# Kernel tuning notes

Hardware: AMD Instinct MI355X
Metric: run time of the kernel (lower is better)

## Reference

```python
import jax, jax.numpy as jnp
import numpy as np

N = 4096
TAU = 0.2          # args.tau relaxation temperature
EPS = 1e-10        # numerical guard for logit of clamped probs


def setup_inputs() -> dict:
    key = jax.random.key(0)
    k1, k2, k3 = jax.random.split(key, 3)
    r = jax.random.uniform(k1, (N, N))
    ori_adj = jnp.where(r < 0.005, -1.0, jnp.where(r < 0.01, 1.0, 0.0)).astype(jnp.float32)
    # nn.init.uniform_(change_links_prob, 0.0, 0.001)
    change_links_prob = jax.random.uniform(k2, (N, N), minval=0.0, maxval=0.001, dtype=jnp.float32)
    # uniform noise for the RelaxedBernoulli logistic reparameterization
    u = jax.random.uniform(k3, (N, N), minval=1e-6, maxval=1.0 - 1e-6, dtype=jnp.float32)
    return {"ori_adj": ori_adj, "change_links_prob": change_links_prob, "u": u}


def reference(ori_adj, change_links_prob, u):
    # --- get_modified_adj: RelaxedBernoulliStraightThrough(tau, clamp(p,0,1)).rsample() ---
    p = jnp.clip(change_links_prob, EPS, 1.0 - EPS)      # torch.clamp(p, 0, 1) + logit guard
    logits = jnp.log(p) - jnp.log1p(-p)
    noise = jnp.log(u) - jnp.log1p(-u)                   # logistic noise
    soft = jax.nn.sigmoid((logits + noise) / TAU)        # relaxed sample
    hard = jnp.round(soft)                               # quantized sample
    change_prob = soft + jax.lax.stop_gradient(hard - soft)  # straight-through
    mod_adj = ori_adj + change_prob * (-2.0 * ori_adj)   # ori_adj * (1 - 2*b)

    # --- balance_degree_directed(mod_adj) ---
    # torch.diag(matrix) returns the diagonal VECTOR, broadcast-subtracted per row (faithful).
    A = mod_adj + mod_adj.T - jnp.diag(mod_adj)
    A_abs = jnp.abs(A)
    tr3 = jnp.einsum('ij,jk,ki->', A, A, A)              # trace(A @ A @ A)
    tr3_abs = jnp.einsum('ij,jk,ki->', A_abs, A_abs, A_abs)
    balance = 0.5 * (1.0 + tr3 / tr3_abs)
    return mod_adj, balance
```

## Files before the change

### kernel.cpp

```cpp
#include <hip/hip_runtime.h>
#include <hip/hip_bf16.h>
#include <cstdint>
#include <cstddef>

#define N 4096
#define NN ((size_t)N * (size_t)N)

typedef int int4v  __attribute__((ext_vector_type(4)));
typedef int int16v __attribute__((ext_vector_type(16)));

__device__ inline void async16(const void* g, void* lds) {
    __builtin_amdgcn_global_load_lds(
        (const __attribute__((address_space(1))) void*)g,
        (__attribute__((address_space(3))) void*)lds, 16, 0, 0);
}

__device__ __noinline__ float mod_full(float p_raw, float uu, float o) {
    float p = fminf(fmaxf(p_raw, 1e-10f), 1.0f - 1e-10f);
    float logits = logf(p) - log1pf(-p);
    float noise  = logf(uu) - log1pf(-uu);
    float y = (logits + noise) / 0.2f;
    float soft = 1.0f / (1.0f + expf(-y));
    float hard = rintf(soft);
    return o + hard * (-2.0f * o);
}

__device__ inline float mod_elem(float p_raw, float uu, float o) {
    float p = fmaxf(p_raw, 1e-10f);
    float s = p + uu;
    if (__builtin_expect(fabsf(s - 1.0f) < 1e-5f, 0))
        return mod_full(p_raw, uu, o);
    return (s > 1.0f) ? -o : o;
}

__global__ void diag_kernel(const float* __restrict__ ori, const float* __restrict__ clp,
                            const float* __restrict__ u, float* __restrict__ diag,
                            double* __restrict__ accs) {
    int j = blockIdx.x * blockDim.x + threadIdx.x;
    size_t idx = (size_t)j * N + j;
    diag[j] = mod_elem(clp[idx], u[idx], ori[idx]);
    if (blockIdx.x == 0 && threadIdx.x < 2) accs[threadIdx.x] = 0.0;
}

__device__ inline int pk4(const int* v) {
    return (v[0] & 255) | ((v[1] & 255) << 8) | ((v[2] & 255) << 16) | ((v[3] & 255) << 24);
}
__device__ inline int pk4a(const int* v) {
    int a0 = v[0] < 0 ? -v[0] : v[0], a1 = v[1] < 0 ? -v[1] : v[1];
    int a2 = v[2] < 0 ? -v[2] : v[2], a3 = v[3] < 0 ? -v[3] : v[3];
    return a0 | (a1 << 8) | (a2 << 16) | (a3 << 24);
}

__global__ __launch_bounds__(256) void fused_mod_A(
        const float* __restrict__ ori, const float* __restrict__ clp,
        const float* __restrict__ u, const float* __restrict__ diag,
        float* __restrict__ out,
        signed char* __restrict__ A, signed char* __restrict__ AT,
        signed char* __restrict__ Aa, signed char* __restrict__ ATa) {
    const int bx = blockIdx.x, by = blockIdx.y;
    if (bx > by) return;
    const bool dg = (bx == by);
    const int bi = bx * 64, bj = by * 64;
    __shared__ float mij[64][68];
    __shared__ float mji[64][68];
    __shared__ float dj_s[64], di_s[64];
    const int t = threadIdx.x;
    const int r = t >> 2;
    const int c16 = (t & 3) << 4;
    if (t < 64) dj_s[t] = diag[bj + t];
    else if (t < 128) di_s[t - 64] = diag[bi + t - 64];
    {
        const size_t base = (size_t)(bi + r) * N + bj + c16;
        #pragma unroll
        for (int q = 0; q < 4; ++q) {
            const size_t idx = base + q * 4;
            float4 p4 = *(const float4*)&clp[idx];
            float4 u4 = *(const float4*)&u[idx];
            float4 o4 = *(const float4*)&ori[idx];
            float4 m4;
            m4.x = mod_elem(p4.x, u4.x, o4.x);
            m4.y = mod_elem(p4.y, u4.y, o4.y);
            m4.z = mod_elem(p4.z, u4.z, o4.z);
            m4.w = mod_elem(p4.w, u4.w, o4.w);
            *(float4*)&out[idx] = m4;
            *(float4*)&mij[r][c16 + q * 4] = m4;
        }
    }
    if (!dg) {
        const size_t base = (size_t)(bj + r) * N + bi + c16;
        #pragma unroll
        for (int q = 0; q < 4; ++q) {
            const size_t idx = base + q * 4;
            float4 p4 = *(const float4*)&clp[idx];
            float4 u4 = *(const float4*)&u[idx];
            float4 o4 = *(const float4*)&ori[idx];
            float4 m4;
            m4.x = mod_elem(p4.x, u4.x, o4.x);
            m4.y = mod_elem(p4.y, u4.y, o4.y);
            m4.z = mod_elem(p4.z, u4.z, o4.z);
            m4.w = mod_elem(p4.w, u4.w, o4.w);
            *(float4*)&out[idx] = m4;
            *(float4*)&mji[r][c16 + q * 4] = m4;
        }
    }
    __syncthreads();
    float (*Mji)[68] = dg ? mij : mji;
    int aF[16], tF[16], aM[16], tM[16];
    const float djr = dj_s[r], dir = di_s[r];
    #pragma unroll
    for (int k = 0; k < 16; ++k) {
        const int c = c16 + k;
        const float x  = mij[r][c];
        const float xt = mij[c][r];
        const float y  = Mji[r][c];
        const float yt = Mji[c][r];
        aF[k] = (int)(x + yt - dj_s[c]);
        tF[k] = (int)(xt + y - djr);
        if (!dg) {
            aM[k] = (int)(y + xt - di_s[c]);
            tM[k] = (int)(yt + x - dir);
        }
    }
    const size_t oF = (size_t)(bi + r) * N + bj + c16;
    const size_t oM = (size_t)(bj + r) * N + bi + c16;
    *(int4*)&A  [oF] = make_int4(pk4 (aF), pk4 (aF + 4), pk4 (aF + 8), pk4 (aF + 12));
    *(int4*)&Aa [oF] = make_int4(pk4a(aF), pk4a(aF + 4), pk4a(aF + 8), pk4a(aF + 12));
    *(int4*)&AT [oM] = make_int4(pk4 (tF), pk4 (tF + 4), pk4 (tF + 8), pk4 (tF + 12));
    *(int4*)&ATa[oM] = make_int4(pk4a(tF), pk4a(tF + 4), pk4a(tF + 8), pk4a(tF + 12));
    if (!dg) {
        *(int4*)&A  [oM] = make_int4(pk4 (aM), pk4 (aM + 4), pk4 (aM + 8), pk4 (aM + 12));
        *(int4*)&Aa [oM] = make_int4(pk4a(aM), pk4a(aM + 4), pk4a(aM + 8), pk4a(aM + 12));
        *(int4*)&AT [oF] = make_int4(pk4 (tM), pk4 (tM + 4), pk4 (tM + 8), pk4 (tM + 12));
        *(int4*)&ATa[oF] = make_int4(pk4a(tM), pk4a(tM + 4), pk4a(tM + 8), pk4a(tM + 12));
    }
}

__global__ __launch_bounds__(256) void gemm_trace_i8(const signed char* __restrict__ Ag,
                                                     const signed char* __restrict__ ATg,
                                                     const signed char* __restrict__ Aag,
                                                     const signed char* __restrict__ ATag,
                                                     double* __restrict__ accs) {
    __shared__ int4v As4[1024];
    __shared__ int4v Bs4[1024];
    __shared__ int red[4];
    const int z = blockIdx.z;
    const signed char* Asrc = z ? Aag  : Ag;
    const signed char* Bsrc = z ? ATag : ATg;
    const int i0 = blockIdx.y * 128;
    const int k0 = blockIdx.x * 128;
    const int t = threadIdx.x;
    const int lane = t & 63;
    const int wave = t >> 6;
    const int wr = (wave >> 1) * 64;
    const int wc = (wave & 1) * 64;
    const int m32 = lane & 31;
    const int kg  = lane >> 5;
    signed char* Asc = (signed char*)As4;
    signed char* Bsc = (signed char*)Bs4;

    const int r0 = t >> 2;
    const int c0 = (t & 3) ^ ((r0 >> 1) & 3);
    const signed char* gA = Asrc + (size_t)(i0 + r0) * N + c0 * 16;
    const signed char* gB = Bsrc + (size_t)(k0 + r0) * N + c0 * 16;
    const int ldst = t * 16;

    int16v acc[2][2];
    #pragma unroll
    for (int a = 0; a < 2; ++a)
        #pragma unroll
        for (int b = 0; b < 2; ++b)
            acc[a][b] = (int16v)(0);

    for (int kb = 0; kb < N; kb += 128) {
        __syncthreads();
        const signed char* ga = gA + kb;
        const signed char* gb = gB + kb;
        async16(ga,               Asc + ldst);
        async16(ga + 64 * N,      Asc + 4096  + ldst);
        async16(ga + 64,          Asc + 8192  + ldst);
        async16(ga + 64 * N + 64, Asc + 12288 + ldst);
        async16(gb,               Bsc + ldst);
        async16(gb + 64 * N,      Bsc + 4096  + ldst);
        async16(gb + 64,          Bsc + 8192  + ldst);
        async16(gb + 64 * N + 64, Bsc + 12288 + ldst);
        __syncthreads();
        #pragma unroll
        for (int half = 0; half < 2; ++half) {
            const int hb = half * 8192;
            #pragma unroll
            for (int q = 0; q < 2; ++q) {
                int4v af[2], bf[2];
                #pragma unroll
                for (int tr = 0; tr < 2; ++tr) {
                    const int row = wr + tr * 32 + m32;
                    const int slot = (q * 2 + kg) ^ ((row >> 1) & 3);
                    af[tr] = *(const int4v*)(Asc + hb + (row << 6) + (slot << 4));
                }
                #pragma unroll
                for (int tc = 0; tc < 2; ++tc) {
                    const int row = wc + tc * 32 + m32;
                    const int slot = (q * 2 + kg) ^ ((row >> 1) & 3);
                    bf[tc] = *(const int4v*)(Bsc + hb + (row << 6) + (slot << 4));
                }
                #pragma unroll
                for (int tr = 0; tr < 2; ++tr)
                    #pragma unroll
                    for (int tc = 0; tc < 2; ++tc)
                        acc[tr][tc] = __builtin_amdgcn_mfma_i32_32x32x32_i8(
                            af[tr], bf[tc], acc[tr][tc], 0, 0, 0);
            }
        }
    }

    int part = 0;
    const int rbase = 4 * kg;
    #pragma unroll
    for (int tr = 0; tr < 2; ++tr) {
        #pragma unroll
        for (int tc = 0; tc < 2; ++tc) {
            const int ib = i0 + wr + tr * 32;
            const int kk = k0 + wc + tc * 32 + m32;
            #pragma unroll
            for (int reg = 0; reg < 16; ++reg) {
                const int row = (reg & 3) + 8 * (reg >> 2) + rbase;
                part += acc[tr][tc][reg] * (int)Bsrc[(size_t)(ib + row) * N + kk];
            }
        }
    }
    #pragma unroll
    for (int off = 32; off > 0; off >>= 1)
        part += __shfl_down(part, off, 64);
    if (lane == 0) red[wave] = part;
    __syncthreads();
    if (t == 0) {
        int tot = red[0] + red[1] + red[2] + red[3];
        atomicAdd(&accs[z], (double)tot);
    }
}

__global__ void finalize_kernel(const double* __restrict__ accs, float* __restrict__ out) {
    out[NN] = (float)(0.5 * (1.0 + accs[0] / accs[1]));
}

extern "C" void kernel_launch(void* const* d_in, const int* in_sizes, int n_in,
                              void* d_out, int out_size, void* d_ws, size_t ws_size,
                              hipStream_t stream) {
    const float* ori = (const float*)d_in[0];
    const float* clp = (const float*)d_in[1];
    const float* u   = (const float*)d_in[2];
    float* out = (float*)d_out;
    char* ws = (char*)d_ws;
    signed char* A8   = (signed char*)ws;
    signed char* AT8  = (signed char*)(ws + NN);
    signed char* Aa8  = (signed char*)(ws + 2 * NN);
    signed char* ATa8 = (signed char*)(ws + 3 * NN);
    float*       diag = (float*)(ws + 4 * NN);
    double*      accs = (double*)(ws + 4 * NN + 4096 * 4);

    diag_kernel<<<dim3(16), 256, 0, stream>>>(ori, clp, u, diag, accs);
    fused_mod_A<<<dim3(N / 64, N / 64), 256, 0, stream>>>(ori, clp, u, diag, out,
                                                          A8, AT8, Aa8, ATa8);
    gemm_trace_i8<<<dim3(N / 128, N / 128, 2), 256, 0, stream>>>(A8, AT8, Aa8, ATa8, accs);
    finalize_kernel<<<1, 1, 0, stream>>>(accs, out);
}
```

Measured before the change: 451.9 us.

## Fold diag and finalize kernels, switch GEMM to 16x16x64 i8 MFMA

Drops the separate diagonal kernel by computing diagonal entries inside each fused_mod_A block, and drops the finalize kernel by having the last GEMM block, found through an atomic ticket counter, compute the balance ratio. The GEMM inner loop moves from 32x32x32 i8 MFMA tiles to 16x16x64 i8 MFMA tiles with a 4x4 accumulator grid and fewer LDS fragment reloads. The mod/A kernel keeps tile values in registers and packs bytes inline, with a padded LDS layout. These changes cut two kernel launches and aim to raise MFMA efficiency, at the cost of redundant diagonal evaluation and a ticket-counter reset that relies on ordering across kernels.

```diff
diff --git a/kernel.cpp b/kernel.cpp
--- a/kernel.cpp
+++ b/kernel.cpp
@@ -6,8 +6,7 @@
 #define N 4096
 #define NN ((size_t)N * (size_t)N)
 
-typedef int int4v  __attribute__((ext_vector_type(4)));
-typedef int int16v __attribute__((ext_vector_type(16)));
+typedef int int4v __attribute__((ext_vector_type(4)));
 
 __device__ inline void async16(const void* g, void* lds) {
     __builtin_amdgcn_global_load_lds(
@@ -33,42 +32,35 @@
     return (s > 1.0f) ? -o : o;
 }
 
-__global__ void diag_kernel(const float* __restrict__ ori, const float* __restrict__ clp,
-                            const float* __restrict__ u, float* __restrict__ diag,
-                            double* __restrict__ accs) {
-    int j = blockIdx.x * blockDim.x + threadIdx.x;
-    size_t idx = (size_t)j * N + j;
-    diag[j] = mod_elem(clp[idx], u[idx], ori[idx]);
-    if (blockIdx.x == 0 && threadIdx.x < 2) accs[threadIdx.x] = 0.0;
-}
-
-__device__ inline int pk4(const int* v) {
-    return (v[0] & 255) | ((v[1] & 255) << 8) | ((v[2] & 255) << 16) | ((v[3] & 255) << 24);
-}
-__device__ inline int pk4a(const int* v) {
-    int a0 = v[0] < 0 ? -v[0] : v[0], a1 = v[1] < 0 ? -v[1] : v[1];
-    int a2 = v[2] < 0 ? -v[2] : v[2], a3 = v[3] < 0 ? -v[3] : v[3];
-    return a0 | (a1 << 8) | (a2 << 16) | (a3 << 24);
-}
-
 __global__ __launch_bounds__(256) void fused_mod_A(
         const float* __restrict__ ori, const float* __restrict__ clp,
-        const float* __restrict__ u, const float* __restrict__ diag,
-        float* __restrict__ out,
+        const float* __restrict__ u, float* __restrict__ out,
         signed char* __restrict__ A, signed char* __restrict__ AT,
-        signed char* __restrict__ Aa, signed char* __restrict__ ATa) {
+        signed char* __restrict__ Aa, signed char* __restrict__ ATa,
+        double* __restrict__ accs) {
     const int bx = blockIdx.x, by = blockIdx.y;
     if (bx > by) return;
     const bool dg = (bx == by);
     const int bi = bx * 64, bj = by * 64;
-    __shared__ float mij[64][68];
-    __shared__ float mji[64][68];
+    __shared__ float mF[64][65];
+    __shared__ float mM[64][65];
     __shared__ float dj_s[64], di_s[64];
     const int t = threadIdx.x;
+    if (bx == 0 && by == 0 && t == 0) {
+        accs[0] = 0.0; accs[1] = 0.0;
+        *(int*)(accs + 2) = 0;
+    }
+    if (t < 64) {
+        size_t jj = (size_t)(bj + t) * N + (bj + t);
+        dj_s[t] = mod_elem(clp[jj], u[jj], ori[jj]);
+    } else if (t < 128) {
+        int q = t - 64;
+        size_t jj = (size_t)(bi + q) * N + (bi + q);
+        di_s[q] = mod_elem(clp[jj], u[jj], ori[jj]);
+    }
     const int r = t >> 2;
     const int c16 = (t & 3) << 4;
-    if (t < 64) dj_s[t] = diag[bj + t];
-    else if (t < 128) di_s[t - 64] = diag[bi + t - 64];
+    float xF[16], xM[16];
     {
         const size_t base = (size_t)(bi + r) * N + bj + c16;
         #pragma unroll
@@ -83,7 +75,8 @@
             m4.z = mod_elem(p4.z, u4.z, o4.z);
             m4.w = mod_elem(p4.w, u4.w, o4.w);
             *(float4*)&out[idx] = m4;
-            *(float4*)&mij[r][c16 + q * 4] = m4;
+            xF[q * 4 + 0] = m4.x; xF[q * 4 + 1] = m4.y;
+            xF[q * 4 + 2] = m4.z; xF[q * 4 + 3] = m4.w;
         }
     }
     if (!dg) {
@@ -100,38 +93,54 @@
             m4.z = mod_elem(p4.z, u4.z, o4.z);
             m4.w = mod_elem(p4.w, u4.w, o4.w);
             *(float4*)&out[idx] = m4;
-            *(float4*)&mji[r][c16 + q * 4] = m4;
-        }
+            xM[q * 4 + 0] = m4.x; xM[q * 4 + 1] = m4.y;
+            xM[q * 4 + 2] = m4.z; xM[q * 4 + 3] = m4.w;
+        }
+    } else {
+        #pragma unroll
+        for (int k = 0; k < 16; ++k) xM[k] = xF[k];
+    }
+    #pragma unroll
+    for (int k = 0; k < 16; ++k) {
+        mF[r][c16 + k] = xF[k];
+        mM[r][c16 + k] = xM[k];
     }
     __syncthreads();
-    float (*Mji)[68] = dg ? mij : mji;
-    int aF[16], tF[16], aM[16], tM[16];
     const float djr = dj_s[r], dir = di_s[r];
+    int pA[4] = {0,0,0,0}, pAa[4] = {0,0,0,0}, pT[4] = {0,0,0,0}, pTa[4] = {0,0,0,0};
+    int qA[4] = {0,0,0,0}, qAa[4] = {0,0,0,0}, qT[4] = {0,0,0,0}, qTa[4] = {0,0,0,0};
     #pragma unroll
     for (int k = 0; k < 16; ++k) {
         const int c = c16 + k;
-        const float x  = mij[r][c];
-        const float xt = mij[c][r];
-        const float y  = Mji[r][c];
-        const float yt = Mji[c][r];
-        aF[k] = (int)(x + yt - dj_s[c]);
-        tF[k] = (int)(xt + y - djr);
+        const float colF = mF[c][r];
+        const float colM = mM[c][r];
+        const int w = k >> 2, sh = (k & 3) * 8;
+        int aF = (int)(xF[k] + colM - dj_s[c]);
+        int tF = (int)(colF + xM[k] - djr);
+        pA [w] |= (aF & 255) << sh;
+        pAa[w] |= (aF < 0 ? -aF : aF) << sh;
+        pT [w] |= (tF & 255) << sh;
+        pTa[w] |= (tF < 0 ? -tF : tF) << sh;
         if (!dg) {
-            aM[k] = (int)(y + xt - di_s[c]);
-            tM[k] = (int)(yt + x - dir);
+            int aM = (int)(xM[k] + colF - di_s[c]);
+            int tM = (int)(colM + xF[k] - dir);
+            qA [w] |= (aM & 255) << sh;
+            qAa[w] |= (aM < 0 ? -aM : aM) << sh;
+            qT [w] |= (tM & 255) << sh;
+            qTa[w] |= (tM < 0 ? -tM : tM) << sh;
         }
     }
     const size_t oF = (size_t)(bi + r) * N + bj + c16;
     const size_t oM = (size_t)(bj + r) * N + bi + c16;
-    *(int4*)&A  [oF] = make_int4(pk4 (aF), pk4 (aF + 4), pk4 (aF + 8), pk4 (aF + 12));
-    *(int4*)&Aa [oF] = make_int4(pk4a(aF), pk4a(aF + 4), pk4a(aF + 8), pk4a(aF + 12));
-    *(int4*)&AT [oM] = make_int4(pk4 (tF), pk4 (tF + 4), pk4 (tF + 8), pk4 (tF + 12));
-    *(int4*)&ATa[oM] = make_int4(pk4a(tF), pk4a(tF + 4), pk4a(tF + 8), pk4a(tF + 12));
+    *(int4*)&A  [oF] = make_int4(pA [0], pA [1], pA [2], pA [3]);
+    *(int4*)&Aa [oF] = make_int4(pAa[0], pAa[1], pAa[2], pAa[3]);
+    *(int4*)&AT [oM] = make_int4(pT [0], pT [1], pT [2], pT [3]);
+    *(int4*)&ATa[oM] = make_int4(pTa[0], pTa[1], pTa[2], pTa[3]);
     if (!dg) {
-        *(int4*)&A  [oM] = make_int4(pk4 (aM), pk4 (aM + 4), pk4 (aM + 8), pk4 (aM + 12));
-        *(int4*)&Aa [oM] = make_int4(pk4a(aM), pk4a(aM + 4), pk4a(aM + 8), pk4a(aM + 12));
-        *(int4*)&AT [oF] = make_int4(pk4 (tM), pk4 (tM + 4), pk4 (tM + 8), pk4 (tM + 12));
-        *(int4*)&ATa[oF] = make_int4(pk4a(tM), pk4a(tM + 4), pk4a(tM + 8), pk4a(tM + 12));
+        *(int4*)&A  [oM] = make_int4(qA [0], qA [1], qA [2], qA [3]);
+        *(int4*)&Aa [oM] = make_int4(qAa[0], qAa[1], qAa[2], qAa[3]);
+        *(int4*)&AT [oF] = make_int4(qT [0], qT [1], qT [2], qT [3]);
+        *(int4*)&ATa[oF] = make_int4(qTa[0], qTa[1], qTa[2], qTa[3]);
     }
 }
 
@@ -139,7 +148,8 @@
                                                      const signed char* __restrict__ ATg,
                                                      const signed char* __restrict__ Aag,
                                                      const signed char* __restrict__ ATag,
-                                                     double* __restrict__ accs) {
+                                                     double* __restrict__ accs,
+                                                     float* __restrict__ out) {
     __shared__ int4v As4[1024];
     __shared__ int4v Bs4[1024];
     __shared__ int red[4];
@@ -151,10 +161,10 @@
     const int t = threadIdx.x;
     const int lane = t & 63;
     const int wave = t >> 6;
+    const int quad = lane >> 4;
+    const int col  = lane & 15;
     const int wr = (wave >> 1) * 64;
     const int wc = (wave & 1) * 64;
-    const int m32 = lane & 31;
-    const int kg  = lane >> 5;
     signed char* Asc = (signed char*)As4;
     signed char* Bsc = (signed char*)Bs4;
 
@@ -164,12 +174,14 @@
     const signed char* gB = Bsrc + (size_t)(k0 + r0) * N + c0 * 16;
     const int ldst = t * 16;
 
-    int16v acc[2][2];
-    #pragma unroll
-    for (int a = 0; a < 2; ++a)
-        #pragma unroll
-        for (int b = 0; b < 2; ++b)
-            acc[a][b] = (int16v)(0);
+    int4v acc[4][4];
+    #pragma unroll
+    for (int a = 0; a < 4; ++a)
+        #pragma unroll
+        for (int b = 0; b < 4; ++b)
+            acc[a][b] = (int4v){0, 0, 0, 0};
+
+    const int fsw = ((quad ^ ((col >> 1) & 3)) << 4);
 
     for (int kb = 0; kb < N; kb += 128) {
         __syncthreads();
@@ -184,47 +196,41 @@
         async16(gb + 64,          Bsc + 8192  + ldst);
         async16(gb + 64 * N + 64, Bsc + 12288 + ldst);
         __syncthreads();
-        #pragma unroll
-        for (int half = 0; half < 2; ++half) {
-            const int hb = half * 8192;
+        int4v af0[4], af1[4], bf0[4], bf1[4];
+        #pragma unroll
+        for (int tr = 0; tr < 4; ++tr) {
+            const int ra = (wr + tr * 16 + col) << 6;
+            af0[tr] = *(const int4v*)(Asc + ra + fsw);
+            af1[tr] = *(const int4v*)(Asc + 8192 + ra + fsw);
+        }
+        #pragma unroll
+        for (int tc = 0; tc < 4; ++tc) {
+            const int rb = (wc + tc * 16 + col) << 6;
+            bf0[tc] = *(const int4v*)(Bsc + rb + fsw);
+            bf1[tc] = *(const int4v*)(Bsc + 8192 + rb + fsw);
+        }
+        #pragma unroll
+        for (int tr = 0; tr < 4; ++tr)
             #pragma unroll
-            for (int q = 0; q < 2; ++q) {
-                int4v af[2], bf[2];
-                #pragma unroll
-                for (int tr = 0; tr < 2; ++tr) {
-                    const int row = wr + tr * 32 + m32;
-                    const int slot = (q * 2 + kg) ^ ((row >> 1) & 3);
-                    af[tr] = *(const int4v*)(Asc + hb + (row << 6) + (slot << 4));
-                }
-                #pragma unroll
-                for (int tc = 0; tc < 2; ++tc) {
-                    const int row = wc + tc * 32 + m32;
-                    const int slot = (q * 2 + kg) ^ ((row >> 1) & 3);
-                    bf[tc] = *(const int4v*)(Bsc + hb + (row << 6) + (slot << 4));
-                }
-                #pragma unroll
-                for (int tr = 0; tr < 2; ++tr)
-                    #pragma unroll
-                    for (int tc = 0; tc < 2; ++tc)
-                        acc[tr][tc] = __builtin_amdgcn_mfma_i32_32x32x32_i8(
-                            af[tr], bf[tc], acc[tr][tc], 0, 0, 0);
-            }
-        }
+            for (int tc = 0; tc < 4; ++tc)
+                acc[tr][tc] = __builtin_amdgcn_mfma_i32_16x16x64_i8(af0[tr], bf0[tc], acc[tr][tc], 0, 0, 0);
+        #pragma unroll
+        for (int tr = 0; tr < 4; ++tr)
+            #pragma unroll
+            for (int tc = 0; tc < 4; ++tc)
+                acc[tr][tc] = __builtin_amdgcn_mfma_i32_16x16x64_i8(af1[tr], bf1[tc], acc[tr][tc], 0, 0, 0);
     }
 
     int part = 0;
-    const int rbase = 4 * kg;
-    #pragma unroll
-    for (int tr = 0; tr < 2; ++tr) {
-        #pragma unroll
-        for (int tc = 0; tc < 2; ++tc) {
-            const int ib = i0 + wr + tr * 32;
-            const int kk = k0 + wc + tc * 32 + m32;
+    #pragma unroll
+    for (int tr = 0; tr < 4; ++tr) {
+        #pragma unroll
+        for (int tc = 0; tc < 4; ++tc) {
+            const int ib = i0 + wr + tr * 16 + quad * 4;
+            const int kk = k0 + wc + tc * 16 + col;
             #pragma unroll
-            for (int reg = 0; reg < 16; ++reg) {
-                const int row = (reg & 3) + 8 * (reg >> 2) + rbase;
-                part += acc[tr][tc][reg] * (int)Bsrc[(size_t)(ib + row) * N + kk];
-            }
+            for (int r = 0; r < 4; ++r)
+                part += acc[tr][tc][r] * (int)Bsrc[(size_t)(ib + r) * N + kk];
         }
     }
     #pragma unroll
@@ -235,11 +241,15 @@
     if (t == 0) {
         int tot = red[0] + red[1] + red[2] + red[3];
         atomicAdd(&accs[z], (double)tot);
-    }
-}
-
-__global__ void finalize_kernel(const double* __restrict__ accs, float* __restrict__ out) {
-    out[NN] = (float)(0.5 * (1.0 + accs[0] / accs[1]));
+        __threadfence();
+        int* done = (int*)(accs + 2);
+        int ticket = atomicAdd(done, 1);
+        if (ticket == 32 * 32 * 2 - 1) {
+            double t3  = atomicAdd(&accs[0], 0.0);
+            double t3a = atomicAdd(&accs[1], 0.0);
+            out[NN] = (float)(0.5 * (1.0 + t3 / t3a));
+        }
+    }
 }
 
 extern "C" void kernel_launch(void* const* d_in, const int* in_sizes, int n_in,
@@ -254,12 +264,9 @@
     signed char* AT8  = (signed char*)(ws + NN);
     signed char* Aa8  = (signed char*)(ws + 2 * NN);
     signed char* ATa8 = (signed char*)(ws + 3 * NN);
-    float*       diag = (float*)(ws + 4 * NN);
-    double*      accs = (double*)(ws + 4 * NN + 4096 * 4);
-
-    diag_kernel<<<dim3(16), 256, 0, stream>>>(ori, clp, u, diag, accs);
-    fused_mod_A<<<dim3(N / 64, N / 64), 256, 0, stream>>>(ori, clp, u, diag, out,
-                                                          A8, AT8, Aa8, ATa8);
-    gemm_trace_i8<<<dim3(N / 128, N / 128, 2), 256, 0, stream>>>(A8, AT8, Aa8, ATa8, accs);
-    finalize_kernel<<<1, 1, 0, stream>>>(accs, out);
-}
+    double*      accs = (double*)(ws + 4 * NN);
+
+    fused_mod_A<<<dim3(N / 64, N / 64), 256, 0, stream>>>(ori, clp, u, out,
+                                                          A8, AT8, Aa8, ATa8, accs);
+    gemm_trace_i8<<<dim3(N / 128, N / 128, 2), 256, 0, stream>>>(A8, AT8, Aa8, ATa8, accs, out);
+}
```

Result: slower. 500.6 us (+10.8%).
